# Kernel optimization log

Measured on AMD Instinct MI355X. Metric: run time of the kernel, lower is better.

Reference implementation:

```python
import jax, jax.numpy as jnp
import numpy as np

N = 100000   # nodes
E = 1600000  # directed edges
F_IN = 100
H = 256
N_LABELS = 19
BN_EPS = 1e-5


def setup_inputs() -> dict:
    key = jax.random.key(0)
    ks = jax.random.split(key, 12)
    p = lambda k, shape, s=0.05: jax.random.normal(k, shape, dtype=jnp.float32) * s
    return {
        "x": jax.random.normal(ks[0], (N, F_IN), dtype=jnp.float32),
        "edge_index": jax.random.randint(ks[1], (2, E), 0, N, dtype=jnp.int32),
        "W1": p(ks[2], (F_IN, F_IN)), "b1": jnp.zeros((F_IN,), jnp.float32),
        "W2": p(ks[3], (F_IN, F_IN)), "b2": jnp.zeros((F_IN,), jnp.float32),
        "W3": p(ks[4], (F_IN, H)),   "b3": jnp.zeros((H,), jnp.float32),
        "fc1_W": p(ks[5], (H, H)),   "fc1_b": jnp.zeros((H,), jnp.float32),
        "fc2a_W": p(ks[6], (H, 128)), "fc2a_b": jnp.zeros((128,), jnp.float32),
        "bn_gamma": jnp.ones((128,), jnp.float32), "bn_beta": jnp.zeros((128,), jnp.float32),
        "fc2b_W": p(ks[7], (128, N_LABELS)), "fc2b_b": jnp.zeros((N_LABELS,), jnp.float32),
    }


def _gcn_conv(x, W, b, src, dst, dinv):
    """PyG GCNConv with add_self_loops + symmetric normalization.
    out[dst] += dinv[src]*dinv[dst] * (x @ W)[src], plus self-loop term, plus bias.
    """
    n = x.shape[0]
    xw = x @ W  # [N, out]
    norm = dinv[src] * dinv[dst]  # [E]
    agg = jax.ops.segment_sum(xw[src] * norm[:, None], dst, num_segments=n)
    agg = agg + xw * (dinv * dinv)[:, None]  # self loops (i -> i)
    return agg + b


def reference(x, edge_index, W1, b1, W2, b2, W3, b3, fc1_W, fc1_b,
              fc2a_W, fc2a_b, bn_gamma, bn_beta, fc2b_W, fc2b_b):
    src, dst = edge_index[0], edge_index[1]
    n = x.shape[0]
    # degree of augmented graph (A + I), computed on targets (sum aggregation)
    deg = jax.ops.segment_sum(jnp.ones((src.shape[0],), x.dtype), dst, num_segments=n) + 1.0
    dinv = jax.lax.rsqrt(deg)

    h = jnp.clip(x, -0.4, 0.4)
    h = jax.nn.relu(_gcn_conv(h, W1, b1, src, dst, dinv))
    h = jax.nn.relu(_gcn_conv(h, W2, b2, src, dst, dinv))
    h = jax.nn.relu(_gcn_conv(h, W3, b3, src, dst, dinv))
    h = jax.nn.relu(h @ fc1_W + fc1_b)
    # fc2: Linear -> BatchNorm1d (train mode, batch stats) -> ReLU -> Linear
    h = h @ fc2a_W + fc2a_b
    mu = jnp.mean(h, axis=0)
    var = jnp.mean(jnp.square(h - mu), axis=0)  # biased var, as torch BN uses
    h = (h - mu) * jax.lax.rsqrt(var + BN_EPS) * bn_gamma + bn_beta
    h = jax.nn.relu(h)
    logits = h @ fc2b_W + fc2b_b
    return jax.nn.log_softmax(logits, axis=1)
```

## Files before the change

kernel.cpp:

```cpp
#include <hip/hip_runtime.h>
#include <hip/hip_bf16.h>

#define N_NODES 100000
#define N_EDGES 1600000
#define F_IN_DIM 100
#define F_IN_PAD 104
#define H_DIM 256
#define BN_DIM 128
#define N_LABELS 19
#define BN_EPS 1e-5f

#define BUCKET_SHIFT 8
#define NB 391
#define EPB 4096
#define PB 391

typedef __attribute__((ext_vector_type(8))) short bf16x8;
typedef __attribute__((ext_vector_type(4))) short s16x4;
typedef __attribute__((ext_vector_type(4))) float f32x4;

static __device__ inline short f2bf(float f) {
    __hip_bfloat16 h = __float2bfloat16(f);
    return *(short*)&h;
}
static __device__ inline float bf2f(short s) {
    unsigned u = ((unsigned)(unsigned short)s) << 16;
    return __builtin_bit_cast(float, u);
}

__global__ __launch_bounds__(256) void part_hist_kernel(const int* __restrict__ dst,
                                                        int* __restrict__ part_hist, int E)
{
    __shared__ int h[NB];
    int tid = threadIdx.x;
    for (int i = tid; i < NB; i += 256) h[i] = 0;
    __syncthreads();
    int base = blockIdx.x * EPB;
    int end = min(base + EPB, E);
    for (int e = base + tid; e < end; e += 256)
        atomicAdd(&h[dst[e] >> BUCKET_SHIFT], 1);
    __syncthreads();
    for (int i = tid; i < NB; i += 256) part_hist[blockIdx.x * NB + i] = h[i];
}

__global__ __launch_bounds__(512) void bucket_total_kernel(const int* __restrict__ part_hist,
                                                           int* __restrict__ bucket_total)
{
    __shared__ int ls[512];
    int b = blockIdx.x;
    int s = 0;
    for (int p = threadIdx.x; p < PB; p += 512) s += part_hist[p * NB + b];
    ls[threadIdx.x] = s;
    __syncthreads();
    for (int off = 256; off > 0; off >>= 1) {
        if (threadIdx.x < off) ls[threadIdx.x] += ls[threadIdx.x + off];
        __syncthreads();
    }
    if (threadIdx.x == 0) bucket_total[b] = ls[0];
}

__global__ __launch_bounds__(512) void bucket_scan_kernel(const int* __restrict__ bucket_total,
                                                          int* __restrict__ bucket_base)
{
    __shared__ int ls[512];
    int tid = threadIdx.x;
    ls[tid] = (tid < NB) ? bucket_total[tid] : 0;
    __syncthreads();
    for (int off = 1; off < 512; off <<= 1) {
        int v = ls[tid];
        int add = (tid >= off) ? ls[tid - off] : 0;
        __syncthreads();
        ls[tid] = v + add;
        __syncthreads();
    }
    if (tid < NB) bucket_base[tid] = (tid > 0) ? ls[tid - 1] : 0;
    if (tid == 0) bucket_base[NB] = ls[NB - 1];
}

__global__ __launch_bounds__(512) void part_offset_kernel(int* __restrict__ part_hist,
                                                          const int* __restrict__ bucket_base)
{
    __shared__ int ls[512];
    int b = blockIdx.x;
    int tid = threadIdx.x;
    int v = (tid < PB) ? part_hist[tid * NB + b] : 0;
    ls[tid] = v;
    __syncthreads();
    for (int off = 1; off < 512; off <<= 1) {
        int x = ls[tid];
        int add = (tid >= off) ? ls[tid - off] : 0;
        __syncthreads();
        ls[tid] = x + add;
        __syncthreads();
    }
    if (tid < PB) part_hist[tid * NB + b] = bucket_base[b] + ((tid > 0) ? ls[tid - 1] : 0);
}

__global__ __launch_bounds__(256) void partition_kernel(const int* __restrict__ src,
                                                        const int* __restrict__ dst,
                                                        const int* __restrict__ part_hist,
                                                        int* __restrict__ ep, int E)
{
    __shared__ int cur[NB];
    int tid = threadIdx.x;
    for (int i = tid; i < NB; i += 256) cur[i] = part_hist[blockIdx.x * NB + i];
    __syncthreads();
    int base = blockIdx.x * EPB;
    int end = min(base + EPB, E);
    for (int e = base + tid; e < end; e += 256) {
        int d = dst[e];
        int s = src[e];
        int pos = atomicAdd(&cur[d >> BUCKET_SHIFT], 1);
        ep[pos] = (s << 8) | (d & 255);
    }
}

__global__ __launch_bounds__(256) void bucket_csr_kernel(const int* __restrict__ ep,
                                                         const int* __restrict__ bucket_base,
                                                         int* __restrict__ row_start,
                                                         float* __restrict__ dinv,
                                                         int* __restrict__ src_sorted, int N, int E)
{
    __shared__ int h[256], sc[256], cur[256];
    int b = blockIdx.x;
    int tid = threadIdx.x;
    int e0 = bucket_base[b], e1 = bucket_base[b + 1];
    int node0 = b << BUCKET_SHIFT;
    int nn = min(256, N - node0);

    h[tid] = 0;
    __syncthreads();
    for (int e = e0 + tid; e < e1; e += 256)
        atomicAdd(&h[ep[e] & 255], 1);
    __syncthreads();

    sc[tid] = h[tid];
    __syncthreads();
    for (int off = 1; off < 256; off <<= 1) {
        int v = sc[tid];
        int add = (tid >= off) ? sc[tid - off] : 0;
        __syncthreads();
        sc[tid] = v + add;
        __syncthreads();
    }
    int excl = e0 + ((tid > 0) ? sc[tid - 1] : 0);
    if (tid < nn) {
        row_start[node0 + tid] = excl;
        dinv[node0 + tid] = rsqrtf((float)h[tid] + 1.0f);
    }
    cur[tid] = excl;
    __syncthreads();
    for (int e = e0 + tid; e < e1; e += 256) {
        int p = ep[e];
        int pos = atomicAdd(&cur[p & 255], 1);
        src_sorted[pos] = ((unsigned)p) >> 8;
    }
    if (b == 0 && tid == 0) row_start[N] = E;
}

__global__ __launch_bounds__(256) void pack_all(
    const float* __restrict__ W1, const float* __restrict__ W2, const float* __restrict__ W3,
    const float* __restrict__ Wf1, const float* __restrict__ Wf2a,
    short* __restrict__ Wt1, short* __restrict__ Wt2, short* __restrict__ Wt3,
    short* __restrict__ Wtf1, short* __restrict__ Wtf2a)
{
    int idx = blockIdx.x * 256 + threadIdx.x;
    const float* W; short* Wt; int K, N, Kp, local;
    if (idx < 10400)       { W = W1;   Wt = Wt1;   K = 100; N = 100; Kp = 104; local = idx; }
    else if (idx < 20800)  { W = W2;   Wt = Wt2;   K = 100; N = 100; Kp = 104; local = idx - 10400; }
    else if (idx < 47424)  { W = W3;   Wt = Wt3;   K = 100; N = 256; Kp = 104; local = idx - 20800; }
    else if (idx < 112960) { W = Wf1;  Wt = Wtf1;  K = 256; N = 256; Kp = 256; local = idx - 47424; }
    else if (idx < 145728) { W = Wf2a; Wt = Wtf2a; K = 256; N = 128; Kp = 256; local = idx - 112960; }
    else return;
    int n = local / Kp, k = local - n * Kp;
    Wt[local] = (k < K) ? f2bf(W[(size_t)k * N + n]) : (short)0;
}

template<int ABF16>
__global__ __launch_bounds__(256) void gemm_oneshot(
    const void* __restrict__ Av, const short* __restrict__ Wt,
    const float* __restrict__ bias, const float* __restrict__ rowscale,
    short* __restrict__ C, int M, int Nout, int strideA, int strideC, int relu)
{
    __shared__ __align__(16) short As[128][F_IN_PAD];
    __shared__ __align__(16) short Bs[128][F_IN_PAD];
    int tid = threadIdx.x;
    int rowBase = blockIdx.x * 128;
    int colBase = blockIdx.y * 128;

    if (ABF16) {
        const short* A = (const short*)Av;
        for (int ch = tid; ch < 128 * 13; ch += 256) {
            int r = ch / 13, c8 = (ch - r * 13) * 8;
            int gr = rowBase + r;
            bf16x8 o = (bf16x8){0,0,0,0,0,0,0,0};
            if (gr < M) o = *(const bf16x8*)(A + (size_t)gr * strideA + c8);
            *(bf16x8*)(&As[r][c8]) = o;
        }
    } else {
        const float* A = (const float*)Av;
        for (int ch = tid; ch < 128 * 25; ch += 256) {
            int r = ch / 25, c4 = (ch - r * 25) * 4;
            int gr = rowBase + r;
            float4 v = make_float4(0.f, 0.f, 0.f, 0.f);
            if (gr < M) v = *(const float4*)(A + (size_t)gr * strideA + c4);
            v.x = fminf(fmaxf(v.x, -0.4f), 0.4f);
            v.y = fminf(fmaxf(v.y, -0.4f), 0.4f);
            v.z = fminf(fmaxf(v.z, -0.4f), 0.4f);
            v.w = fminf(fmaxf(v.w, -0.4f), 0.4f);
            s16x4 o = (s16x4){f2bf(v.x), f2bf(v.y), f2bf(v.z), f2bf(v.w)};
            *(s16x4*)(&As[r][c4]) = o;
        }
        for (int r = tid; r < 128; r += 256)
            *(s16x4*)(&As[r][100]) = (s16x4){0, 0, 0, 0};
    }
    for (int ch = tid; ch < 128 * 13; ch += 256) {
        int n = ch / 13, c8 = (ch - n * 13) * 8;
        int gn = colBase + n;
        bf16x8 o = (bf16x8){0,0,0,0,0,0,0,0};
        if (gn < Nout) o = *(const bf16x8*)(Wt + (size_t)gn * F_IN_PAD + c8);
        *(bf16x8*)(&Bs[n][c8]) = o;
    }
    __syncthreads();

    int wid = tid >> 6;
    int lane = tid & 63;
    int quad = lane >> 4, l15 = lane & 15;
    int wave_m = (wid & 1) * 64;
    int wave_n = (wid >> 1) * 64;

    f32x4 acc[4][4];
    #pragma unroll
    for (int i = 0; i < 4; i++)
        #pragma unroll
        for (int j = 0; j < 4; j++)
            acc[i][j] = (f32x4){0.f, 0.f, 0.f, 0.f};

    #pragma unroll
    for (int kc = 0; kc < 4; kc++) {
        int off = kc * 32 + quad * 8;
        bool ok = (off + 8 <= F_IN_PAD);
        bf16x8 a[4], b[4];
        #pragma unroll
        for (int im = 0; im < 4; im++)
            a[im] = ok ? *(const bf16x8*)(&As[wave_m + im * 16 + l15][off])
                       : (bf16x8){0,0,0,0,0,0,0,0};
        #pragma unroll
        for (int in = 0; in < 4; in++)
            b[in] = ok ? *(const bf16x8*)(&Bs[wave_n + in * 16 + l15][off])
                       : (bf16x8){0,0,0,0,0,0,0,0};
        #pragma unroll
        for (int im = 0; im < 4; im++)
            #pragma unroll
            for (int in = 0; in < 4; in++)
                acc[im][in] = __builtin_amdgcn_mfma_f32_16x16x32_bf16(
                    a[im], b[in], acc[im][in], 0, 0, 0);
    }

    #pragma unroll
    for (int im = 0; im < 4; im++) {
        #pragma unroll
        for (int reg = 0; reg < 4; reg++) {
            int row = rowBase + wave_m + im * 16 + quad * 4 + reg;
            if (row >= M) continue;
            float rs = rowscale ? rowscale[row] : 1.f;
            #pragma unroll
            for (int in = 0; in < 4; in++) {
                int col = colBase + wave_n + in * 16 + l15;
                if (col >= strideC) continue;
                float v = 0.f;
                if (col < Nout) {
                    v = acc[im][in][reg];
                    if (bias) v += bias[col];
                    v *= rs;
                    if (relu) v = fmaxf(v, 0.f);
                }
                C[(size_t)row * strideC + col] = f2bf(v);
            }
        }
    }
}

#define SAP 72
__global__ __launch_bounds__(256) void gemm_mfma(
    const short* __restrict__ A, const short* __restrict__ Wt,
    const float* __restrict__ bias, const float* __restrict__ rowscale,
    short* __restrict__ C, int M, int Kp, int Nout,
    int strideA, int strideC, int relu)
{
    __shared__ __align__(16) short As[128][SAP];
    __shared__ __align__(16) short Bs[128][SAP];

    int tid = threadIdx.x;
    int wid = tid >> 6;
    int lane = tid & 63;
    int quad = lane >> 4;
    int l15 = lane & 15;
    int wave_m = (wid & 1) * 64;
    int wave_n = (wid >> 1) * 64;
    int rowBase = blockIdx.y * 128;
    int colBase = blockIdx.x * 128;

    f32x4 acc[4][4];
    #pragma unroll
    for (int i = 0; i < 4; i++)
        #pragma unroll
        for (int j = 0; j < 4; j++)
            acc[i][j] = (f32x4){0.f, 0.f, 0.f, 0.f};

    bf16x8 pa[4], pb[4];
    int nIter = (Kp + 63) >> 6;

    auto loadA = [&](int k0) {
        #pragma unroll
        for (int i = 0; i < 4; i++) {
            int ch = tid + i * 256;
            int r = ch >> 3, c8 = (ch & 7) << 3;
            int gr = rowBase + r, gk = k0 + c8;
            bf16x8 o = (bf16x8){0,0,0,0,0,0,0,0};
            if (gr < M && gk < strideA)
                o = *(const bf16x8*)(A + (size_t)gr * strideA + gk);
            pa[i] = o;
        }
    };
    auto loadB = [&](int k0) {
        #pragma unroll
        for (int i = 0; i < 4; i++) {
            int ch = tid + i * 256;
            int n = ch >> 3, c8 = (ch & 7) << 3;
            int gn = colBase + n, gk = k0 + c8;
            bf16x8 o = (bf16x8){0,0,0,0,0,0,0,0};
            if (gn < Nout && gk < Kp)
                o = *(const bf16x8*)(Wt + (size_t)gn * Kp + gk);
            pb[i] = o;
        }
    };
    auto storeAB = [&]() {
        #pragma unroll
        for (int i = 0; i < 4; i++) {
            int ch = tid + i * 256;
            int r = ch >> 3, c8 = (ch & 7) << 3;
            *(bf16x8*)(&As[r][c8]) = pa[i];
            *(bf16x8*)(&Bs[r][c8]) = pb[i];
        }
    };

    loadA(0); loadB(0);
    for (int it = 0; it < nIter; ++it) {
        if (it > 0) __syncthreads();
        storeAB();
        __syncthreads();
        if (it + 1 < nIter) { loadA((it + 1) << 6); loadB((it + 1) << 6); }
        #pragma unroll
        for (int ks = 0; ks < 2; ks++) {
            bf16x8 a[4], b[4];
            #pragma unroll
            for (int im = 0; im < 4; im++)
                a[im] = *(const bf16x8*)(&As[wave_m + im * 16 + l15][quad * 8 + ks * 32]);
            #pragma unroll
            for (int in = 0; in < 4; in++)
                b[in] = *(const bf16x8*)(&Bs[wave_n + in * 16 + l15][quad * 8 + ks * 32]);
            #pragma unroll
            for (int im = 0; im < 4; im++)
                #pragma unroll
                for (int in = 0; in < 4; in++)
                    acc[im][in] = __builtin_amdgcn_mfma_f32_16x16x32_bf16(
                        a[im], b[in], acc[im][in], 0, 0, 0);
        }
    }

    #pragma unroll
    for (int im = 0; im < 4; im++) {
        #pragma unroll
        for (int reg = 0; reg < 4; reg++) {
            int row = rowBase + wave_m + im * 16 + quad * 4 + reg;
            if (row >= M) continue;
            float rs = rowscale ? rowscale[row] : 1.f;
            #pragma unroll
            for (int in = 0; in < 4; in++) {
                int col = colBase + wave_n + in * 16 + l15;
                if (col >= strideC) continue;
                float v = 0.f;
                if (col < Nout) {
                    v = acc[im][in][reg];
                    if (bias) v += bias[col];
                    v *= rs;
                    if (relu) v = fmaxf(v, 0.f);
                }
                C[(size_t)row * strideC + col] = f2bf(v);
            }
        }
    }
}

template<int F, int STRIDE, int T, int MODE>
__global__ void gather_kernel(const short* __restrict__ xws,
                              const int* __restrict__ row_start,
                              const int* __restrict__ src_sorted,
                              const float* __restrict__ dinv,
                              const float* __restrict__ bias,
                              short* __restrict__ out, int n)
{
    constexpr int CHUNKS = STRIDE / 8;
    int group = (blockIdx.x * blockDim.x + threadIdx.x) / T;
    int lane = threadIdx.x % T;
    if (group >= n) return;
    int d = group;
    int e0 = row_start[d], e1 = row_start[d + 1];
    bool active = (lane < CHUNKS);
    int coff = lane * 8;
    float acc[8] = {};
    for (int e = e0; e < e1; e++) {
        int s = src_sorted[e];
        if (active) {
            bf16x8 v = *(const bf16x8*)(xws + (size_t)s * STRIDE + coff);
            #pragma unroll
            for (int j = 0; j < 8; j++) acc[j] += bf2f(v[j]);
        }
    }
    if (active) {
        bf16x8 xv = *(const bf16x8*)(xws + (size_t)d * STRIDE + coff);
        float di = dinv[d];
        bf16x8 o;
        #pragma unroll
        for (int j = 0; j < 8; j++) {
            int col = coff + j;
            float v = 0.f;
            if (col < F) {
                v = di * (acc[j] + bf2f(xv[j]));
                if (MODE == 0) v = fmaxf(v + bias[col], 0.f);
                if (MODE == 1) v = di * fmaxf(v + bias[col], 0.f);
            }
            o[j] = f2bf(v);
        }
        *(bf16x8*)(out + (size_t)d * STRIDE + coff) = o;
    }
}

__global__ void bn_stats_kernel(const short* __restrict__ h,
                                float* __restrict__ sum, float* __restrict__ sumsq, int Ntot)
{
    int c = threadIdx.x & 127;
    int rpb = blockDim.x >> 7;
    int r0 = blockIdx.x * rpb + (threadIdx.x >> 7);
    int stride = gridDim.x * rpb;
    float s = 0.f, ss = 0.f;
    for (int r = r0; r < Ntot; r += stride) {
        float v = bf2f(h[(size_t)r * BN_DIM + c]);
        s += v; ss += v * v;
    }
    __shared__ float ls[256], lss[256];
    ls[threadIdx.x] = s; lss[threadIdx.x] = ss;
    __syncthreads();
    if (threadIdx.x < 128) {
        s = ls[threadIdx.x] + ls[threadIdx.x + 128];
        ss = lss[threadIdx.x] + lss[threadIdx.x + 128];
        atomicAdd(&sum[c], s);
        atomicAdd(&sumsq[c], ss);
    }
}

__global__ void bn_finalize_kernel(const float* __restrict__ sum, const float* __restrict__ sumsq,
                                   const float* __restrict__ gamma, const float* __restrict__ beta,
                                   float* __restrict__ a, float* __restrict__ b, int Ntot)
{
    int c = threadIdx.x;
    float inv_n = 1.0f / (float)Ntot;
    float mu = sum[c] * inv_n;
    float var = sumsq[c] * inv_n - mu * mu;
    float ai = gamma[c] * rsqrtf(var + BN_EPS);
    a[c] = ai;
    b[c] = beta[c] - mu * ai;
}

__global__ __launch_bounds__(256) void fc2b_fused_kernel(
    const short* __restrict__ h, const float* __restrict__ bn_a, const float* __restrict__ bn_b,
    const float* __restrict__ W, const float* __restrict__ bias,
    float* __restrict__ out, int Ntot)
{
    __shared__ float Ws[BN_DIM][N_LABELS + 1];
    __shared__ float as[BN_DIM], bs[BN_DIM];
    for (int i = threadIdx.x; i < BN_DIM * N_LABELS; i += 256) {
        int k = i / N_LABELS, j = i - k * N_LABELS;
        Ws[k][j] = W[i];
    }
    if (threadIdx.x < BN_DIM) {
        as[threadIdx.x] = bn_a[threadIdx.x];
        bs[threadIdx.x] = bn_b[threadIdx.x];
    }
    __syncthreads();

    int r = blockIdx.x * 256 + threadIdx.x;
    if (r >= Ntot) return;

    float acc[N_LABELS];
    #pragma unroll
    for (int j = 0; j < N_LABELS; j++) acc[j] = bias[j];

    const short* hr = h + (size_t)r * BN_DIM;
    #pragma unroll
    for (int k0 = 0; k0 < BN_DIM; k0 += 8) {
        bf16x8 hv = *(const bf16x8*)(hr + k0);
        #pragma unroll
        for (int t = 0; t < 8; t++) {
            float v = fmaxf(bf2f(hv[t]) * as[k0 + t] + bs[k0 + t], 0.f);
            #pragma unroll
            for (int j = 0; j < N_LABELS; j++)
                acc[j] = fmaf(v, Ws[k0 + t][j], acc[j]);
        }
    }

    float m = acc[0];
    #pragma unroll
    for (int j = 1; j < N_LABELS; j++) m = fmaxf(m, acc[j]);
    float s = 0.f;
    #pragma unroll
    for (int j = 0; j < N_LABELS; j++) s += expf(acc[j] - m);
    float lse = m + logf(s);
    float* o = out + (size_t)r * N_LABELS;
    #pragma unroll
    for (int j = 0; j < N_LABELS; j++) o[j] = acc[j] - lse;
}

extern "C" void kernel_launch(void* const* d_in, const int* in_sizes, int n_in,
                              void* d_out, int out_size, void* d_ws, size_t ws_size,
                              hipStream_t stream)
{
    const float* x      = (const float*)d_in[0];
    const int*   ei     = (const int*)d_in[1];
    const float* W1     = (const float*)d_in[2];
    const float* b1     = (const float*)d_in[3];
    const float* W2     = (const float*)d_in[4];
    const float* b2     = (const float*)d_in[5];
    const float* W3     = (const float*)d_in[6];
    const float* b3     = (const float*)d_in[7];
    const float* fc1_W  = (const float*)d_in[8];
    const float* fc1_b  = (const float*)d_in[9];
    const float* fc2aW  = (const float*)d_in[10];
    const float* fc2ab  = (const float*)d_in[11];
    const float* gamma  = (const float*)d_in[12];
    const float* beta   = (const float*)d_in[13];
    const float* fc2bW  = (const float*)d_in[14];
    const float* fc2bb  = (const float*)d_in[15];
    float* out = (float*)d_out;

    const int* src = ei;
    const int* dst = ei + N_EDGES;

    char* w = (char*)d_ws;
    float* dinv        = (float*)w;  w += ((size_t)N_NODES * 4 + 255) / 256 * 256;
    int*   row_start   = (int*)w;    w += ((size_t)(N_NODES + 1) * 4 + 255) / 256 * 256;
    int*   part_hist   = (int*)w;    w += ((size_t)PB * NB * 4 + 255) / 256 * 256;
    int*   bucket_total= (int*)w;    w += ((size_t)NB * 4 + 255) / 256 * 256;
    int*   bucket_base = (int*)w;    w += ((size_t)(NB + 1) * 4 + 255) / 256 * 256;
    float* bn_sum      = (float*)w;  w += 128 * 4;
    float* bn_sumsq    = (float*)w;  w += 128 * 4;
    float* bn_a        = (float*)w;  w += 128 * 4;
    float* bn_b        = (float*)w;  w += 128 * 4;
    short* Wt1         = (short*)w;  w += ((size_t)F_IN_DIM * F_IN_PAD * 2 + 255) / 256 * 256;
    short* Wt2         = (short*)w;  w += ((size_t)F_IN_DIM * F_IN_PAD * 2 + 255) / 256 * 256;
    short* Wt3         = (short*)w;  w += ((size_t)H_DIM * F_IN_PAD * 2 + 255) / 256 * 256;
    short* Wtf1        = (short*)w;  w += ((size_t)H_DIM * H_DIM * 2 + 255) / 256 * 256;
    short* Wtf2a       = (short*)w;  w += ((size_t)BN_DIM * H_DIM * 2 + 255) / 256 * 256;
    int*   src_sorted  = (int*)w;    w += ((size_t)N_EDGES * 4 + 255) / 256 * 256;
    int*   ep          = (int*)w;    w += ((size_t)N_EDGES * 4 + 255) / 256 * 256;
    short* xws100      = (short*)w;  w += ((size_t)N_NODES * F_IN_PAD * 2 + 255) / 256 * 256;
    short* agg100      = (short*)w;  w += ((size_t)N_NODES * F_IN_PAD * 2 + 255) / 256 * 256;
    short* big1        = (short*)w;  w += ((size_t)N_NODES * H_DIM * 2 + 255) / 256 * 256;
    short* big2        = (short*)w;  w += ((size_t)N_NODES * H_DIM * 2 + 255) / 256 * 256;

    part_hist_kernel<<<PB, 256, 0, stream>>>(dst, part_hist, N_EDGES);
    bucket_total_kernel<<<NB, 512, 0, stream>>>(part_hist, bucket_total);
    bucket_scan_kernel<<<1, 512, 0, stream>>>(bucket_total, bucket_base);
    part_offset_kernel<<<NB, 512, 0, stream>>>(part_hist, bucket_base);
    partition_kernel<<<PB, 256, 0, stream>>>(src, dst, part_hist, ep, N_EDGES);
    bucket_csr_kernel<<<NB, 256, 0, stream>>>(ep, bucket_base, row_start, dinv,
                                              src_sorted, N_NODES, N_EDGES);

    pack_all<<<570, 256, 0, stream>>>(W1, W2, W3, fc1_W, fc2aW, Wt1, Wt2, Wt3, Wtf1, Wtf2a);

    const int nOne = (N_NODES + 127) / 128;
    int gatherBlocks = (N_NODES * 16 + 255) / 256;

    gemm_oneshot<0><<<dim3(nOne, 1), 256, 0, stream>>>(
        x, Wt1, nullptr, dinv, xws100, N_NODES, F_IN_DIM, F_IN_DIM, F_IN_PAD, 0);
    gather_kernel<F_IN_DIM, F_IN_PAD, 16, 0><<<gatherBlocks, 256, 0, stream>>>(
        xws100, row_start, src_sorted, dinv, b1, agg100, N_NODES);

    gemm_oneshot<1><<<dim3(nOne, 1), 256, 0, stream>>>(
        agg100, Wt2, nullptr, dinv, xws100, N_NODES, F_IN_DIM, F_IN_PAD, F_IN_PAD, 0);
    gather_kernel<F_IN_DIM, F_IN_PAD, 16, 1><<<gatherBlocks, 256, 0, stream>>>(
        xws100, row_start, src_sorted, dinv, b2, agg100, N_NODES);

    gather_kernel<F_IN_DIM, F_IN_PAD, 16, 2><<<gatherBlocks, 256, 0, stream>>>(
        agg100, row_start, src_sorted, dinv, nullptr, xws100, N_NODES);
    gemm_oneshot<1><<<dim3(nOne, 2), 256, 0, stream>>>(
        xws100, Wt3, b3, nullptr, big1, N_NODES, H_DIM, F_IN_PAD, H_DIM, 1);

    gemm_mfma<<<dim3(2, nOne), 256, 0, stream>>>(
        big1, Wtf1, fc1_b, nullptr, big2, N_NODES, H_DIM, H_DIM, H_DIM, H_DIM, 1);

    gemm_mfma<<<dim3(1, nOne), 256, 0, stream>>>(
        big2, Wtf2a, fc2ab, nullptr, big1, N_NODES, H_DIM, BN_DIM, H_DIM, BN_DIM, 0);

    hipMemsetAsync(bn_sum, 0, 2 * 128 * 4, stream);
    bn_stats_kernel<<<512, 256, 0, stream>>>(big1, bn_sum, bn_sumsq, N_NODES);
    bn_finalize_kernel<<<1, 128, 0, stream>>>(bn_sum, bn_sumsq, gamma, beta, bn_a, bn_b, N_NODES);

    fc2b_fused_kernel<<<(N_NODES + 255) / 256, 256, 0, stream>>>(
        big1, bn_a, bn_b, fc2bW, fc2bb, out, N_NODES);
}
```

Before: 732.9 us.

## Fuse fc1 and fc2a GEMMs into one kernel keeping hidden tile in LDS

Replaces the two separate tiled MFMA GEMM launches for fc1 (256->256, ReLU) and fc2a (256->128) with a single kernel. Each 128-row block computes the fc1 output, stores it as bf16 in shared memory, then immediately multiplies it by the fc2a weights, so the 100000x256 intermediate never goes to global memory. Operands are loaded straight from global memory into registers instead of being staged through LDS, and row bounds checks are dropped by padding the buffers to a multiple of 128 rows. The padded tail rows contain uninitialized data that gets computed and written; this looks safe only as long as downstream kernels bound their loops by N.

```diff
diff --git a/kernel.cpp b/kernel.cpp
--- a/kernel.cpp
+++ b/kernel.cpp
@@ -9,6 +9,7 @@
 #define BN_DIM 128
 #define N_LABELS 19
 #define BN_EPS 1e-5f
+#define M_PAD 100096
 
 #define BUCKET_SHIFT 8
 #define NB 391
@@ -281,85 +282,43 @@
     }
 }
 
-#define SAP 72
-__global__ __launch_bounds__(256) void gemm_mfma(
-    const short* __restrict__ A, const short* __restrict__ Wt,
-    const float* __restrict__ bias, const float* __restrict__ rowscale,
-    short* __restrict__ C, int M, int Kp, int Nout,
-    int strideA, int strideC, int relu)
-{
-    __shared__ __align__(16) short As[128][SAP];
-    __shared__ __align__(16) short Bs[128][SAP];
-
+#define HS_PAD 264
+__global__ __launch_bounds__(512, 2) void fc_fused_kernel(
+    const short* __restrict__ A,
+    const short* __restrict__ W1t,
+    const float* __restrict__ b1v,
+    const short* __restrict__ W2t,
+    const float* __restrict__ b2v,
+    short* __restrict__ C)
+{
+    __shared__ __align__(16) short Hs[128][HS_PAD];
     int tid = threadIdx.x;
     int wid = tid >> 6;
     int lane = tid & 63;
-    int quad = lane >> 4;
-    int l15 = lane & 15;
-    int wave_m = (wid & 1) * 64;
-    int wave_n = (wid >> 1) * 64;
-    int rowBase = blockIdx.y * 128;
-    int colBase = blockIdx.x * 128;
-
-    f32x4 acc[4][4];
-    #pragma unroll
-    for (int i = 0; i < 4; i++)
-        #pragma unroll
-        for (int j = 0; j < 4; j++)
-            acc[i][j] = (f32x4){0.f, 0.f, 0.f, 0.f};
-
-    bf16x8 pa[4], pb[4];
-    int nIter = (Kp + 63) >> 6;
-
-    auto loadA = [&](int k0) {
-        #pragma unroll
-        for (int i = 0; i < 4; i++) {
-            int ch = tid + i * 256;
-            int r = ch >> 3, c8 = (ch & 7) << 3;
-            int gr = rowBase + r, gk = k0 + c8;
-            bf16x8 o = (bf16x8){0,0,0,0,0,0,0,0};
-            if (gr < M && gk < strideA)
-                o = *(const bf16x8*)(A + (size_t)gr * strideA + gk);
-            pa[i] = o;
-        }
-    };
-    auto loadB = [&](int k0) {
-        #pragma unroll
-        for (int i = 0; i < 4; i++) {
-            int ch = tid + i * 256;
-            int n = ch >> 3, c8 = (ch & 7) << 3;
-            int gn = colBase + n, gk = k0 + c8;
-            bf16x8 o = (bf16x8){0,0,0,0,0,0,0,0};
-            if (gn < Nout && gk < Kp)
-                o = *(const bf16x8*)(Wt + (size_t)gn * Kp + gk);
-            pb[i] = o;
-        }
-    };
-    auto storeAB = [&]() {
-        #pragma unroll
-        for (int i = 0; i < 4; i++) {
-            int ch = tid + i * 256;
-            int r = ch >> 3, c8 = (ch & 7) << 3;
-            *(bf16x8*)(&As[r][c8]) = pa[i];
-            *(bf16x8*)(&Bs[r][c8]) = pb[i];
-        }
-    };
-
-    loadA(0); loadB(0);
-    for (int it = 0; it < nIter; ++it) {
-        if (it > 0) __syncthreads();
-        storeAB();
-        __syncthreads();
-        if (it + 1 < nIter) { loadA((it + 1) << 6); loadB((it + 1) << 6); }
-        #pragma unroll
-        for (int ks = 0; ks < 2; ks++) {
+    int quad = lane >> 4, l15 = lane & 15;
+    int rowBase = blockIdx.x * 128;
+
+    {
+        int wm = (wid & 1) * 64;
+        int wn = (wid >> 1) * 64;
+        f32x4 acc[4][4];
+        #pragma unroll
+        for (int i = 0; i < 4; i++)
+            #pragma unroll
+            for (int j = 0; j < 4; j++)
+                acc[i][j] = (f32x4){0.f, 0.f, 0.f, 0.f};
+
+        const short* Ab = A + (size_t)(rowBase + wm + l15) * H_DIM + quad * 8;
+        const short* Bb = W1t + (size_t)(wn + l15) * H_DIM + quad * 8;
+        #pragma unroll
+        for (int ks = 0; ks < 8; ks++) {
             bf16x8 a[4], b[4];
             #pragma unroll
             for (int im = 0; im < 4; im++)
-                a[im] = *(const bf16x8*)(&As[wave_m + im * 16 + l15][quad * 8 + ks * 32]);
+                a[im] = *(const bf16x8*)(Ab + (size_t)(im * 16) * H_DIM + ks * 32);
             #pragma unroll
             for (int in = 0; in < 4; in++)
-                b[in] = *(const bf16x8*)(&Bs[wave_n + in * 16 + l15][quad * 8 + ks * 32]);
+                b[in] = *(const bf16x8*)(Bb + (size_t)(in * 16) * H_DIM + ks * 32);
             #pragma unroll
             for (int im = 0; im < 4; im++)
                 #pragma unroll
@@ -367,29 +326,66 @@
                     acc[im][in] = __builtin_amdgcn_mfma_f32_16x16x32_bf16(
                         a[im], b[in], acc[im][in], 0, 0, 0);
         }
-    }
-
-    #pragma unroll
-    for (int im = 0; im < 4; im++) {
-        #pragma unroll
-        for (int reg = 0; reg < 4; reg++) {
-            int row = rowBase + wave_m + im * 16 + quad * 4 + reg;
-            if (row >= M) continue;
-            float rs = rowscale ? rowscale[row] : 1.f;
-            #pragma unroll
-            for (int in = 0; in < 4; in++) {
-                int col = colBase + wave_n + in * 16 + l15;
-                if (col >= strideC) continue;
-                float v = 0.f;
-                if (col < Nout) {
-                    v = acc[im][in][reg];
-                    if (bias) v += bias[col];
-                    v *= rs;
-                    if (relu) v = fmaxf(v, 0.f);
+
+        float bb[4];
+        #pragma unroll
+        for (int in = 0; in < 4; in++) bb[in] = b1v[wn + in * 16 + l15];
+        #pragma unroll
+        for (int im = 0; im < 4; im++)
+            #pragma unroll
+            for (int reg = 0; reg < 4; reg++) {
+                int r = wm + im * 16 + quad * 4 + reg;
+                #pragma unroll
+                for (int in = 0; in < 4; in++) {
+                    int c = wn + in * 16 + l15;
+                    Hs[r][c] = f2bf(fmaxf(acc[im][in][reg] + bb[in], 0.f));
                 }
-                C[(size_t)row * strideC + col] = f2bf(v);
             }
-        }
+    }
+    __syncthreads();
+
+    {
+        int wm = (wid & 1) * 64;
+        int wn = (wid >> 1) * 32;
+        f32x4 acc[4][2];
+        #pragma unroll
+        for (int i = 0; i < 4; i++)
+            #pragma unroll
+            for (int j = 0; j < 2; j++)
+                acc[i][j] = (f32x4){0.f, 0.f, 0.f, 0.f};
+
+        const short* Bb = W2t + (size_t)(wn + l15) * H_DIM + quad * 8;
+        #pragma unroll
+        for (int ks = 0; ks < 8; ks++) {
+            bf16x8 a[4], b[2];
+            #pragma unroll
+            for (int im = 0; im < 4; im++)
+                a[im] = *(const bf16x8*)(&Hs[wm + im * 16 + l15][ks * 32 + quad * 8]);
+            #pragma unroll
+            for (int in = 0; in < 2; in++)
+                b[in] = *(const bf16x8*)(Bb + (size_t)(in * 16) * H_DIM + ks * 32);
+            #pragma unroll
+            for (int im = 0; im < 4; im++)
+                #pragma unroll
+                for (int in = 0; in < 2; in++)
+                    acc[im][in] = __builtin_amdgcn_mfma_f32_16x16x32_bf16(
+                        a[im], b[in], acc[im][in], 0, 0, 0);
+        }
+
+        float bb[2];
+        #pragma unroll
+        for (int in = 0; in < 2; in++) bb[in] = b2v[wn + in * 16 + l15];
+        #pragma unroll
+        for (int im = 0; im < 4; im++)
+            #pragma unroll
+            for (int reg = 0; reg < 4; reg++) {
+                int row = rowBase + wm + im * 16 + quad * 4 + reg;
+                #pragma unroll
+                for (int in = 0; in < 2; in++) {
+                    int col = wn + in * 16 + l15;
+                    C[(size_t)row * BN_DIM + col] = f2bf(acc[im][in][reg] + bb[in]);
+                }
+            }
     }
 }
 
@@ -566,8 +562,8 @@
     int*   ep          = (int*)w;    w += ((size_t)N_EDGES * 4 + 255) / 256 * 256;
     short* xws100      = (short*)w;  w += ((size_t)N_NODES * F_IN_PAD * 2 + 255) / 256 * 256;
     short* agg100      = (short*)w;  w += ((size_t)N_NODES * F_IN_PAD * 2 + 255) / 256 * 256;
-    short* big1        = (short*)w;  w += ((size_t)N_NODES * H_DIM * 2 + 255) / 256 * 256;
-    short* big2        = (short*)w;  w += ((size_t)N_NODES * H_DIM * 2 + 255) / 256 * 256;
+    short* big1        = (short*)w;  w += ((size_t)M_PAD * H_DIM * 2 + 255) / 256 * 256;
+    short* big2        = (short*)w;  w += ((size_t)M_PAD * H_DIM * 2 + 255) / 256 * 256;
 
     part_hist_kernel<<<PB, 256, 0, stream>>>(dst, part_hist, N_EDGES);
     bucket_total_kernel<<<NB, 512, 0, stream>>>(part_hist, bucket_total);
@@ -597,16 +593,13 @@
     gemm_oneshot<1><<<dim3(nOne, 2), 256, 0, stream>>>(
         xws100, Wt3, b3, nullptr, big1, N_NODES, H_DIM, F_IN_PAD, H_DIM, 1);
 
-    gemm_mfma<<<dim3(2, nOne), 256, 0, stream>>>(
-        big1, Wtf1, fc1_b, nullptr, big2, N_NODES, H_DIM, H_DIM, H_DIM, H_DIM, 1);
-
-    gemm_mfma<<<dim3(1, nOne), 256, 0, stream>>>(
-        big2, Wtf2a, fc2ab, nullptr, big1, N_NODES, H_DIM, BN_DIM, H_DIM, BN_DIM, 0);
+    fc_fused_kernel<<<nOne, 512, 0, stream>>>(
+        big1, Wtf1, fc1_b, Wtf2a, fc2ab, big2);
 
     hipMemsetAsync(bn_sum, 0, 2 * 128 * 4, stream);
-    bn_stats_kernel<<<512, 256, 0, stream>>>(big1, bn_sum, bn_sumsq, N_NODES);
+    bn_stats_kernel<<<512, 256, 0, stream>>>(big2, bn_sum, bn_sumsq, N_NODES);
     bn_finalize_kernel<<<1, 128, 0, stream>>>(bn_sum, bn_sumsq, gamma, beta, bn_a, bn_b, N_NODES);
 
     fc2b_fused_kernel<<<(N_NODES + 255) / 256, 256, 0, stream>>>(
-        big1, bn_a, bn_b, fc2bW, fc2bb, out, N_NODES);
-}
+        big2, bn_a, bn_b, fc2bW, fc2bb, out, N_NODES);
+}
```

Result: faster. 670.4 us (-8.5%).
